# Kernel optimization log

Measured on AMD Instinct MI355X. Metric: run time of the kernel, lower is better.

Reference implementation:

```python
import jax, jax.numpy as jnp
import numpy as np

H = 8
D = 512
DK = D // H
B = 16
N = 8192


def setup_inputs() -> dict:
    key = jax.random.key(0)
    k1, k2, k3, k4 = jax.random.split(key, 4)
    x = jax.random.normal(k1, (B, N, D), dtype=jnp.float32)
    W_k = jax.random.normal(k2, (D, D), dtype=jnp.float32) * (1.0 / np.sqrt(D))
    W_g = jax.random.normal(k3, (D, D), dtype=jnp.float32) * (1.0 / np.sqrt(D))
    query = jax.random.normal(k4, (H, 1, DK), dtype=jnp.float32)
    return {"x": x, "W_k": W_k, "W_g": W_g, "query": query}


def reference(x, W_k, W_g, query):
    b, n, d = x.shape
    # nn.Linear: y = x @ W.T  (no bias)
    K = (x @ W_k.T).reshape(b, n, H, DK).transpose(0, 2, 1, 3)  # (b,h,n,dk)
    G = (x @ W_g.T).reshape(b, n, H, DK).transpose(0, 2, 1, 3)  # (b,h,n,dk)
    xh = x.reshape(b, n, H, DK).transpose(0, 2, 1, 3)           # (b,h,n,dk)
    gated = jnp.tanh(K) * jax.nn.sigmoid(G)                     # (b,h,n,dk)
    # single-query attention: scores (b,h,1,n)
    scores = jnp.einsum('hmd,bhnd->bhmn', query, gated)
    attn = jax.nn.softmax(scores, axis=-1)
    out = jnp.einsum('bhmn,bhnd->bhmd', attn, xh)               # (b,h,1,dk)
    out = out.transpose(0, 2, 1, 3).reshape(b, 1, H * DK)
    return out.squeeze()  # (b, d)
```

## Files before the change

### kernel.cpp

```cpp
#include <hip/hip_runtime.h>
#include <hip/hip_bf16.h>

#define H_ 8
#define D_ 512
#define DK_ 64
#define B_ 16
#define N_ 8192
#define M_ (B_ * N_)

typedef __attribute__((ext_vector_type(8))) short short8;
typedef __attribute__((ext_vector_type(4))) float floatx4;

__device__ __forceinline__ void glds16(const void* g, void* l) {
    __builtin_amdgcn_global_load_lds((const __attribute__((address_space(1))) void*)g,
                                     (__attribute__((address_space(3))) void*)l,
                                     16, 0, 0);
}

__device__ __forceinline__ unsigned short f2bf(float f) {
    unsigned u = __float_as_uint(f);
    return (unsigned short)((u + 0x7fffu + ((u >> 16) & 1u)) >> 16);
}

__device__ __forceinline__ unsigned pack_bf2(float x, float y) {
    return __builtin_amdgcn_perm(__float_as_uint(y) + 0x8000u,
                                 __float_as_uint(x) + 0x8000u, 0x07060302u);
}

__device__ __forceinline__ short8 pack_bf8(float4 lo, float4 hi) {
    union { unsigned u[4]; short8 s; } tmp;
    tmp.u[0] = pack_bf2(lo.x, lo.y);
    tmp.u[1] = pack_bf2(lo.z, lo.w);
    tmp.u[2] = pack_bf2(hi.x, hi.y);
    tmp.u[3] = pack_bf2(hi.z, hi.w);
    return tmp.s;
}

__global__ __launch_bounds__(256) void cvt_kernel(const float* __restrict__ src,
                                                  unsigned short* __restrict__ dst, int n4) {
    int i = blockIdx.x * blockDim.x + threadIdx.x;
    int stride = gridDim.x * blockDim.x;
    for (; i < n4; i += stride) {
        float4 v = ((const float4*)src)[i];
        ushort4 o;
        o.x = f2bf(v.x); o.y = f2bf(v.y); o.z = f2bf(v.z); o.w = f2bf(v.w);
        ((ushort4*)dst)[i] = o;
    }
}

__global__ __launch_bounds__(256, 2) void gemm_score_kernel(
    const float* __restrict__ x,
    const unsigned short* __restrict__ wkb,
    const unsigned short* __restrict__ wgb,
    const float* __restrict__ query,
    float* __restrict__ s_buf)
{
    __shared__ unsigned short lds_a[128 * 64];
    __shared__ unsigned short lds_k[128 * 64];
    __shared__ unsigned short lds_g[128 * 64];

    const int t = threadIdx.x;
    const int lane = t & 63;
    const int wave = t >> 6;
    const int wm = wave >> 1, wn = wave & 1;

    const int g = blockIdx.x;
    const int xcd = g & 7;
    const int s = g >> 3;
    const int jt = s & 3;
    const int mt = ((s >> 2) << 3) | xcd;
    const int jc = jt * 128;
    const int m0 = mt * 128;

    floatx4 acc_k[4][4], acc_g[4][4];
#pragma unroll
    for (int i = 0; i < 4; ++i)
#pragma unroll
        for (int j = 0; j < 4; ++j) { acc_k[i][j] = (floatx4)0.f; acc_g[i][j] = (floatx4)0.f; }

    const int r0 = t >> 2;
    const int c0 = t & 3;
    const int swr = ((r0 & 1) << 2) ^ ((r0 >> 1) & 3);
    const float* pA0 = x + (size_t)(m0 + r0) * 512 + c0 * 8;
    const float* pA1 = pA0 + 64 * 512;
    unsigned short* wA00 = lds_a + ((r0 * 8) + (c0 ^ swr)) * 8;
    unsigned short* wA01 = lds_a + ((r0 * 8) + ((c0 ^ swr) ^ 4)) * 8;
    unsigned short* wA10 = wA00 + 64 * 64;
    unsigned short* wA11 = wA01 + 64 * 64;

    int boff[4];
#pragma unroll
    for (int i = 0; i < 4; ++i) {
        int p = i * 256 + t;
        int r = p >> 3;
        int c = (p & 7) ^ (((r & 1) << 2) ^ ((r >> 1) & 3));
        boff[i] = (jc + r) * 512 + c * 8;
    }

    const int fr = lane & 15;
    const int q  = lane >> 4;
    const int swf = ((fr & 1) << 2) ^ ((fr >> 1) & 3);

    for (int k0 = 0; k0 < 512; k0 += 64) {
#pragma unroll
        for (int i = 0; i < 4; ++i) {
            glds16(wkb + boff[i] + k0, lds_k + (size_t)(i * 256 + t) * 8);
            glds16(wgb + boff[i] + k0, lds_g + (size_t)(i * 256 + t) * 8);
        }
        float4 a00 = *(const float4*)(pA0 + k0);
        float4 a01 = *(const float4*)(pA0 + k0 + 4);
        float4 a02 = *(const float4*)(pA0 + k0 + 32);
        float4 a03 = *(const float4*)(pA0 + k0 + 36);
        float4 a10 = *(const float4*)(pA1 + k0);
        float4 a11 = *(const float4*)(pA1 + k0 + 4);
        float4 a12 = *(const float4*)(pA1 + k0 + 32);
        float4 a13 = *(const float4*)(pA1 + k0 + 36);
        *(short8*)wA00 = pack_bf8(a00, a01);
        *(short8*)wA01 = pack_bf8(a02, a03);
        *(short8*)wA10 = pack_bf8(a10, a11);
        *(short8*)wA11 = pack_bf8(a12, a13);
        __syncthreads();

#pragma unroll
        for (int kc = 0; kc < 2; ++kc) {
            const int sl = ((kc * 4 + q) ^ swf) * 8;
            short8 a[4], bk[4], bg[4];
#pragma unroll
            for (int mi = 0; mi < 4; ++mi)
                a[mi] = *(const short8*)(lds_a + (wm * 64 + mi * 16 + fr) * 64 + sl);
#pragma unroll
            for (int ni = 0; ni < 4; ++ni) {
                bk[ni] = *(const short8*)(lds_k + (wn * 64 + ni * 16 + fr) * 64 + sl);
                bg[ni] = *(const short8*)(lds_g + (wn * 64 + ni * 16 + fr) * 64 + sl);
            }
#pragma unroll
            for (int mi = 0; mi < 4; ++mi)
#pragma unroll
                for (int ni = 0; ni < 4; ++ni) {
                    acc_k[mi][ni] = __builtin_amdgcn_mfma_f32_16x16x32_bf16(a[mi], bk[ni], acc_k[mi][ni], 0, 0, 0);
                    acc_g[mi][ni] = __builtin_amdgcn_mfma_f32_16x16x32_bf16(a[mi], bg[ni], acc_g[mi][ni], 0, 0, 0);
                }
        }
        __syncthreads();
    }

    const int h = jt * 2 + wn;
    float qv[4];
#pragma unroll
    for (int ni = 0; ni < 4; ++ni) qv[ni] = query[h * 64 + ni * 16 + fr];

#pragma unroll
    for (int mi = 0; mi < 4; ++mi) {
#pragma unroll
        for (int r = 0; r < 4; ++r) {
            float v = 0.f;
#pragma unroll
            for (int ni = 0; ni < 4; ++ni) {
                float kv = acc_k[mi][ni][r];
                float gv = acc_g[mi][ni][r];
                float e2k = __expf(2.f * kv);
                float th = 1.f - 2.f / (e2k + 1.f);
                float sg = 1.f / (1.f + __expf(-gv));
                v += qv[ni] * th * sg;
            }
            v += __shfl_xor(v, 1);
            v += __shfl_xor(v, 2);
            v += __shfl_xor(v, 4);
            v += __shfl_xor(v, 8);
            if (fr == 0) {
                int mg = m0 + wm * 64 + mi * 16 + (lane >> 4) * 4 + r;
                int b = mg >> 13, n = mg & 8191;
                s_buf[((size_t)(b * 8 + h) << 13) + n] = v;
            }
        }
    }
}

__global__ __launch_bounds__(256) void stats_kernel(const float* __restrict__ s_buf,
                                                    float* __restrict__ mb, float* __restrict__ lb) {
    const int bh = blockIdx.x;
    const float* s = s_buf + ((size_t)bh << 13);
    const int t = threadIdx.x;
    float mx = -3.0e38f;
    for (int i = t; i < 8192; i += 256) mx = fmaxf(mx, s[i]);
#pragma unroll
    for (int m = 32; m > 0; m >>= 1) mx = fmaxf(mx, __shfl_xor(mx, m));
    __shared__ float red[8];
    if ((t & 63) == 0) red[t >> 6] = mx;
    __syncthreads();
    mx = fmaxf(fmaxf(red[0], red[1]), fmaxf(red[2], red[3]));
    float sum = 0.f;
    for (int i = t; i < 8192; i += 256) sum += __expf(s[i] - mx);
#pragma unroll
    for (int m = 32; m > 0; m >>= 1) sum += __shfl_xor(sum, m);
    if ((t & 63) == 0) red[4 + (t >> 6)] = sum;
    __syncthreads();
    if (t == 0) { mb[bh] = mx; lb[bh] = red[4] + red[5] + red[6] + red[7]; }
}

__global__ __launch_bounds__(256) void out_kernel(
    const float* __restrict__ x, const float* __restrict__ s_buf,
    const float* __restrict__ mb, const float* __restrict__ lb,
    float* __restrict__ out) {
    const int b = blockIdx.x >> 5;
    const int chunk = blockIdx.x & 31;
    const int n0 = chunk * 256;
    const int t = threadIdx.x;
    __shared__ float w[8 * 256];
    for (int i = t; i < 2048; i += 256) {
        int hh = i >> 8, nn = i & 255;
        int bh = b * 8 + hh;
        w[i] = __expf(s_buf[((size_t)bh << 13) + n0 + nn] - mb[bh]) / lb[bh];
    }
    __syncthreads();
    const int rg = t >> 6;
    const int d0 = (t & 63) * 8;
    const float* wh = w + ((d0 >> 6) << 8);
    float acc[8] = {0.f, 0.f, 0.f, 0.f, 0.f, 0.f, 0.f, 0.f};
    for (int nn = rg; nn < 256; nn += 4) {
        const float4* row = (const float4*)(x + (((size_t)(b * 8192 + n0 + nn)) << 9) + d0);
        float4 v0 = row[0];
        float4 v1 = row[1];
        float ww = wh[nn];
        acc[0] += ww * v0.x; acc[1] += ww * v0.y;
        acc[2] += ww * v0.z; acc[3] += ww * v0.w;
        acc[4] += ww * v1.x; acc[5] += ww * v1.y;
        acc[6] += ww * v1.z; acc[7] += ww * v1.w;
    }
#pragma unroll
    for (int j = 0; j < 8; ++j) atomicAdd(&out[b * 512 + d0 + j], acc[j]);
}

extern "C" void kernel_launch(void* const* d_in, const int* in_sizes, int n_in,
                              void* d_out, int out_size, void* d_ws, size_t ws_size,
                              hipStream_t stream) {
    const float* x  = (const float*)d_in[0];
    const float* Wk = (const float*)d_in[1];
    const float* Wg = (const float*)d_in[2];
    const float* q  = (const float*)d_in[3];
    float* out = (float*)d_out;

    char* ws = (char*)d_ws;
    unsigned short* wkb = (unsigned short*)ws;
    unsigned short* wgb = (unsigned short*)(ws + 524288ull);
    float* s_buf = (float*)(ws + 1048576ull);
    float* mb = (float*)(ws + 5242880ull);
    float* lb = (float*)(ws + 5243392ull);

    hipMemsetAsync(d_out, 0, 512 * B_ * sizeof(float), stream);

    hipLaunchKernelGGL(cvt_kernel, dim3(256), dim3(256), 0, stream, Wk, wkb, (D_ * D_) / 4);
    hipLaunchKernelGGL(cvt_kernel, dim3(256), dim3(256), 0, stream, Wg, wgb, (D_ * D_) / 4);
    hipLaunchKernelGGL(gemm_score_kernel, dim3(4096), dim3(256), 0, stream, x, wkb, wgb, q, s_buf);
    hipLaunchKernelGGL(stats_kernel, dim3(128), dim3(256), 0, stream, s_buf, mb, lb);
    hipLaunchKernelGGL(out_kernel, dim3(512), dim3(256), 0, stream, x, s_buf, mb, lb, out);
}
```

Before: 584.7 us.

## Double-buffer GEMM LDS tiles with K=32 steps and replace atomics with partial-sum reduce

```diff
diff --git a/kernel.cpp b/kernel.cpp
--- a/kernel.cpp
+++ b/kernel.cpp
@@ -36,16 +36,18 @@
     return tmp.s;
 }
 
-__global__ __launch_bounds__(256) void cvt_kernel(const float* __restrict__ src,
-                                                  unsigned short* __restrict__ dst, int n4) {
-    int i = blockIdx.x * blockDim.x + threadIdx.x;
-    int stride = gridDim.x * blockDim.x;
-    for (; i < n4; i += stride) {
-        float4 v = ((const float4*)src)[i];
-        ushort4 o;
-        o.x = f2bf(v.x); o.y = f2bf(v.y); o.z = f2bf(v.z); o.w = f2bf(v.w);
-        ((ushort4*)dst)[i] = o;
-    }
+__global__ __launch_bounds__(256) void cvt2_kernel(const float* __restrict__ s0,
+                                                   const float* __restrict__ s1,
+                                                   unsigned short* __restrict__ d0,
+                                                   unsigned short* __restrict__ d1) {
+    const int blk = blockIdx.x;
+    const float* src = (blk < 256) ? s0 : s1;
+    unsigned short* dst = (blk < 256) ? d0 : d1;
+    int i = (blk & 255) * 256 + threadIdx.x;
+    float4 v = ((const float4*)src)[i];
+    ushort4 o;
+    o.x = f2bf(v.x); o.y = f2bf(v.y); o.z = f2bf(v.z); o.w = f2bf(v.w);
+    ((ushort4*)dst)[i] = o;
 }
 
 __global__ __launch_bounds__(256, 2) void gemm_score_kernel(
@@ -55,9 +57,7 @@
     const float* __restrict__ query,
     float* __restrict__ s_buf)
 {
-    __shared__ unsigned short lds_a[128 * 64];
-    __shared__ unsigned short lds_k[128 * 64];
-    __shared__ unsigned short lds_g[128 * 64];
+    __shared__ unsigned short lds[6][128 * 32];
 
     const int t = threadIdx.x;
     const int lane = t & 63;
@@ -78,70 +78,80 @@
 #pragma unroll
         for (int j = 0; j < 4; ++j) { acc_k[i][j] = (floatx4)0.f; acc_g[i][j] = (floatx4)0.f; }
 
-    const int r0 = t >> 2;
-    const int c0 = t & 3;
-    const int swr = ((r0 & 1) << 2) ^ ((r0 >> 1) & 3);
-    const float* pA0 = x + (size_t)(m0 + r0) * 512 + c0 * 8;
-    const float* pA1 = pA0 + 64 * 512;
-    unsigned short* wA00 = lds_a + ((r0 * 8) + (c0 ^ swr)) * 8;
-    unsigned short* wA01 = lds_a + ((r0 * 8) + ((c0 ^ swr) ^ 4)) * 8;
-    unsigned short* wA10 = wA00 + 64 * 64;
-    unsigned short* wA11 = wA01 + 64 * 64;
-
-    int boff[4];
-#pragma unroll
-    for (int i = 0; i < 4; ++i) {
+    const int ar = t >> 1;
+    const int ac0 = (t & 1) * 2;
+    const int aswr = (ar >> 1) & 3;
+    const float* pA = x + (size_t)(m0 + ar) * 512 + (t & 1) * 16;
+    const int ao0 = (ar * 4 + (ac0 ^ aswr)) * 8;
+    const int ao1 = (ar * 4 + ((ac0 + 1) ^ aswr)) * 8;
+
+    int boff[2];
+#pragma unroll
+    for (int i = 0; i < 2; ++i) {
         int p = i * 256 + t;
-        int r = p >> 3;
-        int c = (p & 7) ^ (((r & 1) << 2) ^ ((r >> 1) & 3));
+        int r = p >> 2;
+        int c = (p & 3) ^ ((r >> 1) & 3);
         boff[i] = (jc + r) * 512 + c * 8;
     }
 
     const int fr = lane & 15;
     const int q  = lane >> 4;
-    const int swf = ((fr & 1) << 2) ^ ((fr >> 1) & 3);
-
-    for (int k0 = 0; k0 < 512; k0 += 64) {
-#pragma unroll
-        for (int i = 0; i < 4; ++i) {
-            glds16(wkb + boff[i] + k0, lds_k + (size_t)(i * 256 + t) * 8);
-            glds16(wgb + boff[i] + k0, lds_g + (size_t)(i * 256 + t) * 8);
-        }
-        float4 a00 = *(const float4*)(pA0 + k0);
-        float4 a01 = *(const float4*)(pA0 + k0 + 4);
-        float4 a02 = *(const float4*)(pA0 + k0 + 32);
-        float4 a03 = *(const float4*)(pA0 + k0 + 36);
-        float4 a10 = *(const float4*)(pA1 + k0);
-        float4 a11 = *(const float4*)(pA1 + k0 + 4);
-        float4 a12 = *(const float4*)(pA1 + k0 + 32);
-        float4 a13 = *(const float4*)(pA1 + k0 + 36);
-        *(short8*)wA00 = pack_bf8(a00, a01);
-        *(short8*)wA01 = pack_bf8(a02, a03);
-        *(short8*)wA10 = pack_bf8(a10, a11);
-        *(short8*)wA11 = pack_bf8(a12, a13);
-        __syncthreads();
-
-#pragma unroll
-        for (int kc = 0; kc < 2; ++kc) {
-            const int sl = ((kc * 4 + q) ^ swf) * 8;
-            short8 a[4], bk[4], bg[4];
-#pragma unroll
-            for (int mi = 0; mi < 4; ++mi)
-                a[mi] = *(const short8*)(lds_a + (wm * 64 + mi * 16 + fr) * 64 + sl);
+    const int slq = (q ^ ((fr >> 1) & 3)) * 8;
+
+#pragma unroll
+    for (int i = 0; i < 2; ++i) {
+        glds16(wkb + boff[i], &lds[2][(i * 256 + t) * 8]);
+        glds16(wgb + boff[i], &lds[4][(i * 256 + t) * 8]);
+    }
+    {
+        float4 f0 = *(const float4*)(pA + 0);
+        float4 f1 = *(const float4*)(pA + 4);
+        float4 f2 = *(const float4*)(pA + 8);
+        float4 f3 = *(const float4*)(pA + 12);
+        *(short8*)&lds[0][ao0] = pack_bf8(f0, f1);
+        *(short8*)&lds[0][ao1] = pack_bf8(f2, f3);
+    }
+    __syncthreads();
+
+#pragma unroll
+    for (int k = 0; k < 16; ++k) {
+        const int cur = k & 1, nxt = cur ^ 1;
+        float4 f0, f1, f2, f3;
+        if (k < 15) {
+            const int k1 = (k + 1) * 32;
+#pragma unroll
+            for (int i = 0; i < 2; ++i) {
+                glds16(wkb + boff[i] + k1, &lds[2 + nxt][(i * 256 + t) * 8]);
+                glds16(wgb + boff[i] + k1, &lds[4 + nxt][(i * 256 + t) * 8]);
+            }
+            f0 = *(const float4*)(pA + k1 + 0);
+            f1 = *(const float4*)(pA + k1 + 4);
+            f2 = *(const float4*)(pA + k1 + 8);
+            f3 = *(const float4*)(pA + k1 + 12);
+        }
+
+        short8 a[4], bk[4], bg[4];
+#pragma unroll
+        for (int mi = 0; mi < 4; ++mi)
+            a[mi] = *(const short8*)(&lds[cur][(wm * 64 + mi * 16 + fr) * 32 + slq]);
+#pragma unroll
+        for (int ni = 0; ni < 4; ++ni) {
+            bk[ni] = *(const short8*)(&lds[2 + cur][(wn * 64 + ni * 16 + fr) * 32 + slq]);
+            bg[ni] = *(const short8*)(&lds[4 + cur][(wn * 64 + ni * 16 + fr) * 32 + slq]);
+        }
+#pragma unroll
+        for (int mi = 0; mi < 4; ++mi)
 #pragma unroll
             for (int ni = 0; ni < 4; ++ni) {
-                bk[ni] = *(const short8*)(lds_k + (wn * 64 + ni * 16 + fr) * 64 + sl);
-                bg[ni] = *(const short8*)(lds_g + (wn * 64 + ni * 16 + fr) * 64 + sl);
-            }
-#pragma unroll
-            for (int mi = 0; mi < 4; ++mi)
-#pragma unroll
-                for (int ni = 0; ni < 4; ++ni) {
-                    acc_k[mi][ni] = __builtin_amdgcn_mfma_f32_16x16x32_bf16(a[mi], bk[ni], acc_k[mi][ni], 0, 0, 0);
-                    acc_g[mi][ni] = __builtin_amdgcn_mfma_f32_16x16x32_bf16(a[mi], bg[ni], acc_g[mi][ni], 0, 0, 0);
-                }
-        }
-        __syncthreads();
+                acc_k[mi][ni] = __builtin_amdgcn_mfma_f32_16x16x32_bf16(a[mi], bk[ni], acc_k[mi][ni], 0, 0, 0);
+                acc_g[mi][ni] = __builtin_amdgcn_mfma_f32_16x16x32_bf16(a[mi], bg[ni], acc_g[mi][ni], 0, 0, 0);
+            }
+
+        if (k < 15) {
+            *(short8*)&lds[nxt][ao0] = pack_bf8(f0, f1);
+            *(short8*)&lds[nxt][ao1] = pack_bf8(f2, f3);
+            __syncthreads();
+        }
     }
 
     const int h = jt * 2 + wn;
@@ -198,10 +208,10 @@
     if (t == 0) { mb[bh] = mx; lb[bh] = red[4] + red[5] + red[6] + red[7]; }
 }
 
-__global__ __launch_bounds__(256) void out_kernel(
+__global__ __launch_bounds__(256) void out_part_kernel(
     const float* __restrict__ x, const float* __restrict__ s_buf,
     const float* __restrict__ mb, const float* __restrict__ lb,
-    float* __restrict__ out) {
+    float* __restrict__ part) {
     const int b = blockIdx.x >> 5;
     const int chunk = blockIdx.x & 31;
     const int n0 = chunk * 256;
@@ -227,8 +237,19 @@
         acc[4] += ww * v1.x; acc[5] += ww * v1.y;
         acc[6] += ww * v1.z; acc[7] += ww * v1.w;
     }
-#pragma unroll
-    for (int j = 0; j < 8; ++j) atomicAdd(&out[b * 512 + d0 + j], acc[j]);
+    float* dst = part + ((size_t)(blockIdx.x * 4 + rg)) * 512 + d0;
+    *(float4*)(dst)     = make_float4(acc[0], acc[1], acc[2], acc[3]);
+    *(float4*)(dst + 4) = make_float4(acc[4], acc[5], acc[6], acc[7]);
+}
+
+__global__ __launch_bounds__(512) void out_reduce_kernel(const float* __restrict__ part,
+                                                         float* __restrict__ out) {
+    const int b = blockIdx.x;
+    const int d = threadIdx.x;
+    float s = 0.f;
+    const float* p = part + (size_t)b * 128 * 512 + d;
+    for (int i = 0; i < 128; ++i) s += p[(size_t)i * 512];
+    out[b * 512 + d] = s;
 }
 
 extern "C" void kernel_launch(void* const* d_in, const int* in_sizes, int n_in,
@@ -244,14 +265,13 @@
     unsigned short* wkb = (unsigned short*)ws;
     unsigned short* wgb = (unsigned short*)(ws + 524288ull);
     float* s_buf = (float*)(ws + 1048576ull);
-    float* mb = (float*)(ws + 5242880ull);
-    float* lb = (float*)(ws + 5243392ull);
-
-    hipMemsetAsync(d_out, 0, 512 * B_ * sizeof(float), stream);
-
-    hipLaunchKernelGGL(cvt_kernel, dim3(256), dim3(256), 0, stream, Wk, wkb, (D_ * D_) / 4);
-    hipLaunchKernelGGL(cvt_kernel, dim3(256), dim3(256), 0, stream, Wg, wgb, (D_ * D_) / 4);
+    float* part  = (float*)(ws + 5242880ull);
+    float* mb = (float*)(ws + 9437184ull);
+    float* lb = (float*)(ws + 9437696ull);
+
+    hipLaunchKernelGGL(cvt2_kernel, dim3(512), dim3(256), 0, stream, Wk, Wg, wkb, wgb);
     hipLaunchKernelGGL(gemm_score_kernel, dim3(4096), dim3(256), 0, stream, x, wkb, wgb, q, s_buf);
     hipLaunchKernelGGL(stats_kernel, dim3(128), dim3(256), 0, stream, s_buf, mb, lb);
-    hipLaunchKernelGGL(out_kernel, dim3(512), dim3(256), 0, stream, x, s_buf, mb, lb, out);
-}
+    hipLaunchKernelGGL(out_part_kernel, dim3(512), dim3(256), 0, stream, x, s_buf, mb, lb, part);
+    hipLaunchKernelGGL(out_reduce_kernel, dim3(16), dim3(512), 0, stream, part, out);
+}
```

After: 621.5 us. +6.3%, slower.
